# Kernel tuning notes

Measured on AMD Instinct MI355X. Metric: run time of the kernel, lower is better.

Reference implementation:

```python
import jax, jax.numpy as jnp
import numpy as np

T = 16384      # sentence_len
D_IN = 1024    # input_size (== 2*H, so SRU uses k=3 with split-highway)
H = 512        # hidden_size per direction
NC = 15        # n_classes


def setup_inputs() -> dict:
    key = jax.random.key(0)
    ks = jax.random.split(key, 16)

    def w(k, shape, fan):
        return jax.random.normal(k, shape, jnp.float32) / np.float32(np.sqrt(fan))

    inp = {
        "x": jax.random.normal(ks[0], (T, D_IN), jnp.float32),
        # layer 0 (input D_IN), forward + backward directions
        "w0f": w(ks[1], (D_IN, 3 * H), D_IN), "v0f": w(ks[2], (2, H), H), "b0f": jnp.zeros((2, H), jnp.float32),
        "w0b": w(ks[3], (D_IN, 3 * H), D_IN), "v0b": w(ks[4], (2, H), H), "b0b": jnp.zeros((2, H), jnp.float32),
        # layer 1 (input 2*H == D_IN)
        "w1f": w(ks[5], (2 * H, 3 * H), 2 * H), "v1f": w(ks[6], (2, H), H), "b1f": jnp.zeros((2, H), jnp.float32),
        "w1b": w(ks[7], (2 * H, 3 * H), 2 * H), "v1b": w(ks[8], (2, H), H), "b1b": jnp.zeros((2, H), jnp.float32),
        # classification head
        "fc_w": w(ks[9], (2 * H, NC), 2 * H), "fc_b": jnp.zeros((NC,), jnp.float32),
    }
    return inp


def _sru_dir(x_in, x_res, W, v, b, reverse):
    """One SRU direction. x_in: [T, d_in], x_res: [T, H] highway input.
    SRU v2 cell (sru library CUDA kernel, activation=identity):
      g1 = sigma(U1 + vf*c_prev + bf);  c = g1*c_prev + (1-g1)*U0
      g2 = sigma(U2 + vr*c      + br);  h = g2*c + (1-g2)*x_res
    """
    h_dim = v.shape[1]
    U = x_in @ W                                   # [T, 3H]
    u0, u1, u2 = U[:, :h_dim], U[:, h_dim:2 * h_dim], U[:, 2 * h_dim:]
    vf, vr = v[0], v[1]
    bf, br = b[0], b[1]

    def step(c, ins):
        u0t, u1t, u2t, xrt = ins
        g1 = jax.nn.sigmoid(u1t + vf * c + bf)
        c_new = g1 * c + (1.0 - g1) * u0t
        g2 = jax.nn.sigmoid(u2t + vr * c_new + br)
        h = g2 * c_new + (1.0 - g2) * xrt
        return c_new, h

    c0 = jnp.zeros((h_dim,), x_in.dtype)
    _, hs = jax.lax.scan(step, c0, (u0, u1, u2, x_res), reverse=reverse)
    return hs                                       # [T, H]


def _sru_layer(x, wf, vf, bf, wb, vb, bb):
    # bidirectional; input dim == 2H so each direction's highway uses its half of x
    hf = _sru_dir(x, x[:, :H], wf, vf, bf, reverse=False)
    hb = _sru_dir(x, x[:, H:], wb, vb, bb, reverse=True)
    return jnp.concatenate([hf, hb], axis=-1)       # [T, 2H]


def reference(x, w0f, v0f, b0f, w0b, v0b, b0b,
              w1f, v1f, b1f, w1b, v1b, b1b, fc_w, fc_b):
    h = _sru_layer(x, w0f, v0f, b0f, w0b, v0b, b0b)
    h = _sru_layer(h, w1f, v1f, b1f, w1b, v1b, b1b)
    return h @ fc_w + fc_b                          # [T, NC]
```

## Files before the change

kernel.cpp:

```cpp
#include <hip/hip_runtime.h>


#define T_LEN 16384
#define D_IN 1024
#define HDIM 512
#define NC 15
#define NU2 3072
#define CHUNK 64
#define WARM 64
#define NCHUNK (T_LEN / CHUNK)
#define L2E 1.44269504f

typedef __attribute__((ext_vector_type(8))) short short8v;
typedef __attribute__((ext_vector_type(4))) float float4v;
typedef __attribute__((ext_vector_type(4))) int int4v;

__device__ __forceinline__ unsigned short f2bf(float f) {
    unsigned u = __float_as_uint(f);
    unsigned r = (u + 0x7FFFu + ((u >> 16) & 1u)) >> 16;
    return (unsigned short)r;
}
__device__ __forceinline__ float bf2f(unsigned s) {
    return __uint_as_float(s << 16);
}
__device__ __forceinline__ float sigm2(float zarg) {
    float e = __builtin_amdgcn_exp2f(zarg);
    return __builtin_amdgcn_rcpf(1.0f + e);
}

#define GLDS(gp, lp)                                                          \
    __builtin_amdgcn_global_load_lds(                                         \
        (const __attribute__((address_space(1))) unsigned int*)(gp),          \
        (__attribute__((address_space(3))) unsigned int*)(lp), 16, 0, 0)

__global__ __launch_bounds__(256) void cast_f32_bf16(const float* __restrict__ in,
                                                     unsigned short* __restrict__ out,
                                                     long n) {
    long i = ((long)blockIdx.x * blockDim.x + threadIdx.x) * 4;
    if (i + 3 < n) {
        float4v v = *(const float4v*)(in + i);
        unsigned short o0 = f2bf(v[0]), o1 = f2bf(v[1]), o2 = f2bf(v[2]), o3 = f2bf(v[3]);
        unsigned short* p = out + i;
        p[0] = o0; p[1] = o1; p[2] = o2; p[3] = o3;
    }
}

__global__ __launch_bounds__(256) void transpose_perm4(const float* __restrict__ w0f,
                                                       const float* __restrict__ w0b,
                                                       const float* __restrict__ w1f,
                                                       const float* __restrict__ w1b,
                                                       unsigned short* __restrict__ wt0,
                                                       unsigned short* __restrict__ wt1) {
    __shared__ float tile[32][33];
    const int K = 1024, N = 1536;
    int z = blockIdx.z;
    const float* w = (z == 0) ? w0f : (z == 1) ? w0b : (z == 2) ? w1f : w1b;
    unsigned short* wt = (z < 2) ? wt0 : wt1;
    if (z & 1) wt += (size_t)1536 * K;

    int n0 = blockIdx.x * 32, k0 = blockIdx.y * 32;
    int tx = threadIdx.x;
    int ty = threadIdx.y;
    int sc;
    if (n0 < 1024) sc = (tx >> 4) * 512 + (n0 >> 1) + (tx & 15);
    else           sc = n0 + tx;
#pragma unroll
    for (int i = 0; i < 32; i += 8)
        tile[ty + i][tx] = w[(size_t)(k0 + ty + i) * N + sc];
    __syncthreads();
#pragma unroll
    for (int i = 0; i < 32; i += 8)
        wt[(size_t)(n0 + ty + i) * K + k0 + tx] = f2bf(tile[tx][ty + i]);
}

#define GBM 256
#define GBN 256
#define GBK 32
#define SLOT_B 32768

__global__ __launch_bounds__(512, 2) void gemm_pipe(const unsigned short* __restrict__ A,
                                                    const unsigned short* __restrict__ Bt,
                                                    unsigned* __restrict__ P01F,
                                                    unsigned short* __restrict__ P2F,
                                                    unsigned* __restrict__ P01B,
                                                    unsigned short* __restrict__ P2B,
                                                    const float* __restrict__ bias_f,
                                                    const float* __restrict__ bias_b) {
    extern __shared__ char smem[];
    const int K = 1024;

    int tid = threadIdx.x;
    int h = blockIdx.x;
    int w = (h & 7) * 96 + (h >> 3);
    int xcd = w / 96, lw = w % 96;
    int m0 = (xcd * 8 + (lw & 7)) * GBM;
    int n0 = (lw >> 3) * GBN;

    int wid = tid >> 6, lane = tid & 63;
    int wr = wid >> 2, wc = wid & 3;
    int l15 = lane & 15, l4 = lane >> 4;

    int rr = tid >> 2;
    int cs = (((tid & 3) ^ (rr & 3) ^ ((rr >> 2) & 3)) << 3);
    size_t asrc = (size_t)(m0 + rr) * K + cs;
    size_t bsrc = (size_t)(n0 + rr) * K + cs;
    int ldst = wid << 10;

    int chko = ((l4 ^ (l15 & 3) ^ ((l15 >> 2) & 3)) << 4);
    int base_a = (wr * 128 + l15) * 64 + chko;
    int base_b = 16384 + (wc * 64 + l15) * 64 + chko;

#pragma unroll
    for (int t = 0; t < 2; ++t) {
        char* sb = smem + t * SLOT_B;
        GLDS(A + asrc + (size_t)t * GBK, sb + ldst);
        GLDS(A + asrc + (size_t)128 * K + (size_t)t * GBK, sb + 8192 + ldst);
        GLDS(Bt + bsrc + (size_t)t * GBK, sb + 16384 + ldst);
        GLDS(Bt + bsrc + (size_t)128 * K + (size_t)t * GBK, sb + 16384 + 8192 + ldst);
    }

    float4v acc[8][4] = {};
    short8v bfr[4], af[4];

    for (int t = 0; t < 32; ++t) {
        asm volatile("s_waitcnt vmcnt(4)" ::: "memory");
        __builtin_amdgcn_s_barrier();
        char* sb = smem + (t & 3) * SLOT_B;
        int tn = (t + 2) & 31;
        char* sn = smem + (tn & 3) * SLOT_B;

#pragma unroll
        for (int n = 0; n < 4; ++n)
            bfr[n] = *(const short8v*)(sb + base_b + n * 1024);
#pragma unroll
        for (int m = 0; m < 4; ++m)
            af[m] = *(const short8v*)(sb + base_a + m * 1024);
        GLDS(A + asrc + (size_t)tn * GBK, sn + ldst);
        GLDS(A + asrc + (size_t)128 * K + (size_t)tn * GBK, sn + 8192 + ldst);
        __builtin_amdgcn_s_setprio(1);
#pragma unroll
        for (int m = 0; m < 4; ++m)
#pragma unroll
            for (int n = 0; n < 4; ++n)
                acc[m][n] = __builtin_amdgcn_mfma_f32_16x16x32_bf16(
                    af[m], bfr[n], acc[m][n], 0, 0, 0);
        __builtin_amdgcn_s_setprio(0);
        __builtin_amdgcn_s_barrier();

#pragma unroll
        for (int m = 0; m < 4; ++m)
            af[m] = *(const short8v*)(sb + base_a + (m + 4) * 1024);
        GLDS(Bt + bsrc + (size_t)tn * GBK, sn + 16384 + ldst);
        GLDS(Bt + bsrc + (size_t)128 * K + (size_t)tn * GBK, sn + 16384 + 8192 + ldst);
        __builtin_amdgcn_s_setprio(1);
#pragma unroll
        for (int m = 0; m < 4; ++m)
#pragma unroll
            for (int n = 0; n < 4; ++n)
                acc[m + 4][n] = __builtin_amdgcn_mfma_f32_16x16x32_bf16(
                    af[m], bfr[n], acc[m + 4][n], 0, 0, 0);
        __builtin_amdgcn_s_setprio(0);
    }

    int sec = (n0 >= 1536) ? 1 : 0;
    int nX = n0 - sec * 1536;
    const float* bias = sec ? bias_b : bias_f;

    if (nX < 1024) {
        unsigned* dst = sec ? P01B : P01F;
#pragma unroll
        for (int fp = 0; fp < 2; ++fp) {
            int ch = (nX >> 1) + wc * 32 + fp * 16 + l15;
            float bv = -L2E * bias[ch];
#pragma unroll
            for (int fm = 0; fm < 8; ++fm) {
                int r0 = m0 + wr * 128 + fm * 16 + l4 * 4;
#pragma unroll
                for (int j = 0; j < 4; ++j) {
                    unsigned lo = f2bf(acc[fm][2 * fp][j]);
                    unsigned hi = f2bf(fmaf(-L2E, acc[fm][2 * fp + 1][j], bv));
                    dst[(size_t)(r0 + j) * 512 + ch] = lo | (hi << 16);
                }
            }
        }
    } else {
        unsigned short* dst = sec ? P2B : P2F;
#pragma unroll
        for (int fn = 0; fn < 4; ++fn) {
            int ch = (nX - 1024) + wc * 64 + fn * 16 + l15;
            float bv = -L2E * bias[512 + ch];
#pragma unroll
            for (int fm = 0; fm < 8; ++fm) {
                int r0 = m0 + wr * 128 + fm * 16 + l4 * 4;
#pragma unroll
                for (int j = 0; j < 4; ++j)
                    dst[(size_t)(r0 + j) * 512 + ch] =
                        f2bf(fmaf(-L2E, acc[fm][fn][j], bv));
            }
        }
    }
}

#define DM 16
#define DW 8
__global__ __launch_bounds__(256, 4) void sru_scan(
        const unsigned* __restrict__ P01f, const unsigned short* __restrict__ P2f,
        const unsigned* __restrict__ P01b, const unsigned short* __restrict__ P2b,
        const unsigned short* __restrict__ xrf, const unsigned short* __restrict__ xrb,
        const float* __restrict__ vF, const float* __restrict__ vB,
        unsigned short* __restrict__ hout) {
    int dir = blockIdx.z;
    int ch = blockIdx.x * 64 + threadIdx.x;
    int cid = blockIdx.y * 4 + threadIdx.y;

    const unsigned* P01;
    const unsigned short *P2, *xr;
    const float* vv;
    int outc;
    if (dir == 0) { P01 = P01f; P2 = P2f; xr = xrf; vv = vF; outc = ch; }
    else          { P01 = P01b; P2 = P2b; xr = xrb; vv = vB; outc = HDIM + ch; }

    float vfs = -L2E * vv[ch];
    float vrs = -L2E * vv[HDIM + ch];

    int cb = cid * CHUNK;
    int tstep = dir ? -1 : 1;
    int mstart = dir ? cb + CHUNK - 1 : cb;
    int wstart, wn;
    if (dir == 0) {
        wstart = cb - WARM; if (wstart < 0) wstart = 0;
        wn = cb - wstart;
    } else {
        wstart = cb + CHUNK - 1 + WARM; if (wstart > T_LEN - 1) wstart = T_LEN - 1;
        wn = wstart - (cb + CHUNK - 1);
    }

    unsigned wr_[DW];
#pragma unroll
    for (int d = 0; d < DW; d++) {
        if (d < wn) {
            int t = wstart + tstep * d;
            wr_[d] = P01[(unsigned)t * 512u + ch];
        }
    }
    unsigned a01[DM], a2[DM], axr[DM];
#pragma unroll
    for (int d = 0; d < DM; d++) {
        int t = mstart + tstep * d;
        unsigned bi = (unsigned)t * 512u + ch;
        a01[d] = P01[bi]; a2[d] = P2[bi];
        axr[d] = xr[(unsigned)t * 1024u + ch];
    }

    float c = 0.0f;
    for (int nb = 0; nb < wn; nb += DW) {
#pragma unroll
        for (int d = 0; d < DW; d++) {
            int n = nb + d;
            if (n < wn) {
                unsigned p = wr_[d];
                float u0 = bf2f(p << 16 >> 16);
                float u1s = __uint_as_float(p & 0xffff0000u);
                int np = n + DW;
                if (np < wn) {
                    int tp = wstart + tstep * np;
                    wr_[d] = P01[(unsigned)tp * 512u + ch];
                }
                float g1 = sigm2(fmaf(vfs, c, u1s));
                c = u0 + g1 * (c - u0);
            }
        }
    }
    for (int nb = 0; nb < CHUNK; nb += DM) {
#pragma unroll
        for (int d = 0; d < DM; d++) {
            int n = nb + d;
            int t = mstart + tstep * n;
            unsigned p = a01[d];
            float u0 = bf2f(p << 16 >> 16);
            float u1s = __uint_as_float(p & 0xffff0000u);
            float u2s = bf2f(a2[d]);
            float xv = bf2f(axr[d]);
            int np = n + DM;
            if (np < CHUNK) {
                int tp = mstart + tstep * np;
                unsigned bi = (unsigned)tp * 512u + ch;
                a01[d] = P01[bi]; a2[d] = P2[bi];
                axr[d] = xr[(unsigned)tp * 1024u + ch];
            }
            float g1 = sigm2(fmaf(vfs, c, u1s));
            c = u0 + g1 * (c - u0);
            float g2 = sigm2(fmaf(vrs, c, u2s));
            float h = xv + g2 * (c - xv);
            hout[(unsigned)t * 1024u + outc] = f2bf(h);
        }
    }
}

__global__ __launch_bounds__(256) void fc_kernel(const unsigned short* __restrict__ h,
                                                 const float* __restrict__ W,
                                                 const float* __restrict__ bias,
                                                 float* __restrict__ out) {
    int gwid = (int)((blockIdx.x * (size_t)blockDim.x + threadIdx.x) >> 6);
    int lane = threadIdx.x & 63;
    int r0 = gwid * 4;
    int k0 = lane * 16;

    float hv[4][16];
#pragma unroll
    for (int r = 0; r < 4; r++) {
#pragma unroll
        for (int i = 0; i < 16; i += 8) {
            short8v v = *(const short8v*)(h + (size_t)(r0 + r) * D_IN + k0 + i);
#pragma unroll
            for (int j = 0; j < 8; j++)
                hv[r][i + j] = bf2f((unsigned short)v[j]);
        }
    }
    float acc[4][NC];
#pragma unroll
    for (int r = 0; r < 4; r++)
#pragma unroll
        for (int cdx = 0; cdx < NC; cdx++) acc[r][cdx] = 0.0f;

#pragma unroll
    for (int i = 0; i < 16; i++) {
        const float* wrow = W + (size_t)(k0 + i) * NC;
#pragma unroll
        for (int cdx = 0; cdx < NC; cdx++) {
            float wv = wrow[cdx];
            acc[0][cdx] += hv[0][i] * wv;
            acc[1][cdx] += hv[1][i] * wv;
            acc[2][cdx] += hv[2][i] * wv;
            acc[3][cdx] += hv[3][i] * wv;
        }
    }
#pragma unroll
    for (int r = 0; r < 4; r++)
#pragma unroll
        for (int cdx = 0; cdx < NC; cdx++) {
            float s = acc[r][cdx];
#pragma unroll
            for (int m = 1; m < 64; m <<= 1) s += __shfl_xor(s, m, 64);
            acc[r][cdx] = s;
        }
#pragma unroll
    for (int r = 0; r < 4; r++) {
        float val = 0.0f;
#pragma unroll
        for (int cdx = 0; cdx < NC; cdx++)
            if (lane == cdx) val = acc[r][cdx];
        if (lane < NC) out[(size_t)(r0 + r) * NC + lane] = val + bias[lane];
    }
}

extern "C" void kernel_launch(void* const* d_in, const int* in_sizes, int n_in,
                              void* d_out, int out_size, void* d_ws, size_t ws_size,
                              hipStream_t stream) {
    const float* x    = (const float*)d_in[0];
    const float* w0f  = (const float*)d_in[1];
    const float* v0f  = (const float*)d_in[2];
    const float* b0f  = (const float*)d_in[3];
    const float* w0b  = (const float*)d_in[4];
    const float* v0b  = (const float*)d_in[5];
    const float* b0b  = (const float*)d_in[6];
    const float* w1f  = (const float*)d_in[7];
    const float* v1f  = (const float*)d_in[8];
    const float* b1f  = (const float*)d_in[9];
    const float* w1b  = (const float*)d_in[10];
    const float* v1b  = (const float*)d_in[11];
    const float* b1b  = (const float*)d_in[12];
    const float* fcw  = (const float*)d_in[13];
    const float* fcb  = (const float*)d_in[14];
    float* out = (float*)d_out;

    char* ws = (char*)d_ws;
    const size_t XB_B  = (size_t)T_LEN * D_IN * 2;
    const size_t WT_B  = (size_t)NU2 * D_IN * 2;
    const size_t H0_B  = (size_t)T_LEN * D_IN * 2;
    const size_t P01_B = (size_t)T_LEN * HDIM * 4;
    const size_t P2_B  = (size_t)T_LEN * HDIM * 2;

    size_t off = 0;
    unsigned short* xb   = (unsigned short*)(ws + off); off += XB_B;
    unsigned short* h1   = xb;
    unsigned short* wt0  = (unsigned short*)(ws + off); off += WT_B;
    unsigned short* wt1  = (unsigned short*)(ws + off); off += WT_B;
    unsigned short* h0   = (unsigned short*)(ws + off); off += H0_B;
    unsigned*       P01F = (unsigned*)(ws + off);       off += P01_B;
    unsigned short* P2F  = (unsigned short*)(ws + off); off += P2_B;
    unsigned*       P01B = (unsigned*)(ws + off);       off += P01_B;
    unsigned short* P2B  = (unsigned short*)(ws + off); off += P2_B;

    cast_f32_bf16<<<T_LEN * D_IN / 4 / 256, 256, 0, stream>>>(x, xb, (long)T_LEN * D_IN);
    dim3 tb(32, 8);
    dim3 tg(1536 / 32, D_IN / 32, 4);
    transpose_perm4<<<tg, tb, 0, stream>>>(w0f, w0b, w1f, w1b, wt0, wt1);

    dim3 gg((T_LEN / GBM) * (NU2 / GBN));
    dim3 sg(HDIM / 64, NCHUNK / 4, 2);
    dim3 sb(64, 4, 1);

    gemm_pipe<<<gg, 512, 4 * SLOT_B, stream>>>(xb, wt0, P01F, P2F, P01B, P2B, b0f, b0b);
    sru_scan<<<sg, sb, 0, stream>>>(P01F, P2F, P01B, P2B,
                                    xb, xb + HDIM, v0f, v0b, h0);

    gemm_pipe<<<gg, 512, 4 * SLOT_B, stream>>>(h0, wt1, P01F, P2F, P01B, P2B, b1f, b1b);
    sru_scan<<<sg, sb, 0, stream>>>(P01F, P2F, P01B, P2B,
                                    h0, h0 + HDIM, v1f, v1b, h1);

    fc_kernel<<<T_LEN / 4 * 64 / 256, 256, 0, stream>>>(h1, fcw, fcb, out);
    (void)in_sizes; (void)n_in; (void)out_size;
}
```

Baseline: 353.2 us.

## Pack four timesteps of u2 per channel into 64-bit words and halve scan chunk

The GEMM epilogue now writes the u2 gate projection as 64-bit words holding four consecutive timesteps per channel, and the scan loads one 64-bit word per four steps instead of four 16-bit loads. This cuts the number of narrow scattered stores and loads for the P2 buffer. CHUNK also drops from 64 to 32, which doubles the number of scan chunks for more parallelism, but the fixed 64-step warmup now covers a larger share of each chunk's work. The reverse direction extracts the packed halves in reversed order.

```diff
diff --git a/kernel.cpp b/kernel.cpp
--- a/kernel.cpp
+++ b/kernel.cpp
@@ -6,7 +6,7 @@
 #define HDIM 512
 #define NC 15
 #define NU2 3072
-#define CHUNK 64
+#define CHUNK 32
 #define WARM 64
 #define NCHUNK (T_LEN / CHUNK)
 #define L2E 1.44269504f
@@ -81,9 +81,9 @@
 __global__ __launch_bounds__(512, 2) void gemm_pipe(const unsigned short* __restrict__ A,
                                                     const unsigned short* __restrict__ Bt,
                                                     unsigned* __restrict__ P01F,
-                                                    unsigned short* __restrict__ P2F,
+                                                    unsigned long long* __restrict__ P2F,
                                                     unsigned* __restrict__ P01B,
-                                                    unsigned short* __restrict__ P2B,
+                                                    unsigned long long* __restrict__ P2B,
                                                     const float* __restrict__ bias_f,
                                                     const float* __restrict__ bias_b) {
     extern __shared__ char smem[];
@@ -184,7 +184,7 @@
             }
         }
     } else {
-        unsigned short* dst = sec ? P2B : P2F;
+        unsigned long long* dst = sec ? P2B : P2F;
 #pragma unroll
         for (int fn = 0; fn < 4; ++fn) {
             int ch = (nX - 1024) + wc * 64 + fn * 16 + l15;
@@ -192,10 +192,12 @@
 #pragma unroll
             for (int fm = 0; fm < 8; ++fm) {
                 int r0 = m0 + wr * 128 + fm * 16 + l4 * 4;
+                unsigned long long v = 0;
 #pragma unroll
                 for (int j = 0; j < 4; ++j)
-                    dst[(size_t)(r0 + j) * 512 + ch] =
-                        f2bf(fmaf(-L2E, acc[fm][fn][j], bv));
+                    v |= (unsigned long long)f2bf(fmaf(-L2E, acc[fm][fn][j], bv))
+                         << (16 * j);
+                dst[(size_t)(r0 >> 2) * 512 + ch] = v;
             }
         }
     }
@@ -204,8 +206,8 @@
 #define DM 16
 #define DW 8
 __global__ __launch_bounds__(256, 4) void sru_scan(
-        const unsigned* __restrict__ P01f, const unsigned short* __restrict__ P2f,
-        const unsigned* __restrict__ P01b, const unsigned short* __restrict__ P2b,
+        const unsigned* __restrict__ P01f, const unsigned long long* __restrict__ P2f,
+        const unsigned* __restrict__ P01b, const unsigned long long* __restrict__ P2b,
         const unsigned short* __restrict__ xrf, const unsigned short* __restrict__ xrb,
         const float* __restrict__ vF, const float* __restrict__ vB,
         unsigned short* __restrict__ hout) {
@@ -214,11 +216,12 @@
     int cid = blockIdx.y * 4 + threadIdx.y;
 
     const unsigned* P01;
-    const unsigned short *P2, *xr;
+    const unsigned long long* P2q;
+    const unsigned short* xr;
     const float* vv;
     int outc;
-    if (dir == 0) { P01 = P01f; P2 = P2f; xr = xrf; vv = vF; outc = ch; }
-    else          { P01 = P01b; P2 = P2b; xr = xrb; vv = vB; outc = HDIM + ch; }
+    if (dir == 0) { P01 = P01f; P2q = P2f; xr = xrf; vv = vF; outc = ch; }
+    else          { P01 = P01b; P2q = P2b; xr = xrb; vv = vB; outc = HDIM + ch; }
 
     float vfs = -L2E * vv[ch];
     float vrs = -L2E * vv[HDIM + ch];
@@ -243,12 +246,17 @@
             wr_[d] = P01[(unsigned)t * 512u + ch];
         }
     }
-    unsigned a01[DM], a2[DM], axr[DM];
+    unsigned a01[DM], axr[DM];
+    unsigned long long a2q[DM / 4];
+#pragma unroll
+    for (int s = 0; s < DM / 4; s++) {
+        int tg = mstart + tstep * (s * 4);
+        a2q[s] = P2q[((unsigned)tg >> 2) * 512u + ch];
+    }
 #pragma unroll
     for (int d = 0; d < DM; d++) {
         int t = mstart + tstep * d;
-        unsigned bi = (unsigned)t * 512u + ch;
-        a01[d] = P01[bi]; a2[d] = P2[bi];
+        a01[d] = P01[(unsigned)t * 512u + ch];
         axr[d] = xr[(unsigned)t * 1024u + ch];
     }
 
@@ -271,21 +279,31 @@
             }
         }
     }
+    unsigned long long g2cur = 0;
     for (int nb = 0; nb < CHUNK; nb += DM) {
 #pragma unroll
         for (int d = 0; d < DM; d++) {
             int n = nb + d;
             int t = mstart + tstep * n;
+            if ((d & 3) == 0) {
+                g2cur = a2q[d >> 2];
+                int np16 = n + DM;
+                if (np16 < CHUNK) {
+                    int tg = mstart + tstep * np16;
+                    a2q[d >> 2] = P2q[((unsigned)tg >> 2) * 512u + ch];
+                }
+            }
             unsigned p = a01[d];
             float u0 = bf2f(p << 16 >> 16);
             float u1s = __uint_as_float(p & 0xffff0000u);
-            float u2s = bf2f(a2[d]);
+            int hh = dir ? (3 - (d & 3)) : (d & 3);
+            float u2s = bf2f((unsigned)(g2cur >> (16 * hh)) & 0xffffu);
             float xv = bf2f(axr[d]);
             int np = n + DM;
             if (np < CHUNK) {
                 int tp = mstart + tstep * np;
                 unsigned bi = (unsigned)tp * 512u + ch;
-                a01[d] = P01[bi]; a2[d] = P2[bi];
+                a01[d] = P01[bi];
                 axr[d] = xr[(unsigned)tp * 1024u + ch];
             }
             float g1 = sigm2(fmaf(vfs, c, u1s));
@@ -388,9 +406,9 @@
     unsigned short* wt1  = (unsigned short*)(ws + off); off += WT_B;
     unsigned short* h0   = (unsigned short*)(ws + off); off += H0_B;
     unsigned*       P01F = (unsigned*)(ws + off);       off += P01_B;
-    unsigned short* P2F  = (unsigned short*)(ws + off); off += P2_B;
+    unsigned long long* P2F = (unsigned long long*)(ws + off); off += P2_B;
     unsigned*       P01B = (unsigned*)(ws + off);       off += P01_B;
-    unsigned short* P2B  = (unsigned short*)(ws + off); off += P2_B;
+    unsigned long long* P2B = (unsigned long long*)(ws + off); off += P2_B;
 
     cast_f32_bf16<<<T_LEN * D_IN / 4 / 256, 256, 0, stream>>>(x, xb, (long)T_LEN * D_IN);
     dim3 tb(32, 8);
```

After: 384.2 us. 8.8% more time.
